# Kernel optimization log

Measured on AMD Instinct MI355X. Metric: run time of the kernel, lower is better.

## Reference

```python
import jax, jax.numpy as jnp
import numpy as np

N = 32768          # total proposals (batch of images concatenated)
C = 81             # num classes (class 0 = background)
K = 4096           # fixed candidate budget for masked NMS (jit-friendly)
SCORE_THRESH = 0.05
NMS_THRESH = 0.5
IMG_W, IMG_H = 1333.0, 800.0   # image size for clip_to_image
CLS_OFFSET = 4096.0            # > max coord: offsets boxes per label so NMS is per-class


def setup_inputs() -> dict:
    key = jax.random.key(0)
    k1, k2, k3 = jax.random.split(key, 3)
    x = jax.random.normal(k1, (N, C), dtype=jnp.float32)
    xy = jax.random.uniform(k2, (N, 2), dtype=jnp.float32) * jnp.array([IMG_W * 0.9, IMG_H * 0.9], jnp.float32)
    wh = 4.0 + jax.random.uniform(k3, (N, 2), dtype=jnp.float32) * 124.0
    boxes = jnp.concatenate([xy, xy + wh], axis=-1)  # [N,4] xyxy
    return {"x": x, "boxes": boxes}


def _pairwise_iou(b):
    # b: [K,4] xyxy -> [K,K] IoU
    x1, y1, x2, y2 = b[:, 0], b[:, 1], b[:, 2], b[:, 3]
    area = (x2 - x1) * (y2 - y1)
    iw = jnp.maximum(jnp.minimum(x2[:, None], x2[None, :]) - jnp.maximum(x1[:, None], x1[None, :]), 0.0)
    ih = jnp.maximum(jnp.minimum(y2[:, None], y2[None, :]) - jnp.maximum(y1[:, None], y1[None, :]), 0.0)
    inter = iw * ih
    return inter / (area[:, None] + area[None, :] - inter + 1e-9)


def reference(x, boxes):
    # softmax scores
    prob = jax.nn.softmax(x, axis=-1)                    # [N,C]
    # clip_to_image (remove_empty=False)
    bx = jnp.stack([
        jnp.clip(boxes[:, 0], 0.0, IMG_W - 1),
        jnp.clip(boxes[:, 1], 0.0, IMG_H - 1),
        jnp.clip(boxes[:, 2], 0.0, IMG_W - 1),
        jnp.clip(boxes[:, 3], 0.0, IMG_H - 1)], axis=-1)  # [N,4]
    # score threshold + drop background (label 0), as in filter_results
    valid = (prob > SCORE_THRESH) & (jnp.arange(C)[None, :] != 0)
    flat = jnp.where(valid, prob, -1.0).reshape(-1)       # [N*C]
    vals, idx = jax.lax.top_k(flat, K)                    # sorted desc
    box_idx = idx // C
    labels = idx % C                                      # [K] int
    bk = bx[box_idx]                                      # [K,4] (boxes repeated per class in torch code)
    keep0 = vals > 0.0                                    # invalid slots padded with -1
    # multi-label NMS: offset boxes by label so different classes never overlap
    boff = bk + (labels.astype(bk.dtype) * CLS_OFFSET)[:, None]
    iou_gt = _pairwise_iou(boff) > NMS_THRESH             # [K,K] bool
    order = jnp.arange(K)

    def step(keep, i):
        sup = keep[i] & (order > i) & iou_gt[i]
        return keep & ~sup, None

    keep, _ = jax.lax.scan(step, keep0, order)
    dets = jnp.where(keep[:, None],
                     jnp.concatenate([bk, vals[:, None]], axis=-1),
                     0.0)                                 # [K,5] = xyxy + score
    return dets, labels, keep
```

## Files before the change

kernel.cpp:

```cpp
#include <hip/hip_runtime.h>

#pragma clang fp contract(off)

typedef unsigned int u32;
typedef unsigned long long u64;
typedef long long i64;

#define N_ROWS 32768
#define NCLS 81
#define TOPK 4096
#define MAXCAND 327680
#define SELCAP 12288
#define IMGW_M1 1332.0f
#define IMGH_M1 799.0f

#define CAND_THREADS 256
#define RPB 32
#define CAND_GRID (N_ROWS / RPB)
#define CPT 11
#define BLK_CAND_CAP 640
#define ROW_F4 ((RPB * NCLS) / 4)

#define H1_BASE 0x3D4Cu
#define H1_BINS 576
#define H1_SLICES 64

#define COLL_GRID 512
#define SEG_LDS 4096

#define MCAP 1024
#define MMAX 512
#define NW32 16

__device__ inline double fast_exp_neg(double d) {
    if (d < -45.0) return 0.0;
    const double L2E    = 1.4426950408889634074;
    const double LN2_HI = 6.93147180369123816490e-01;
    const double LN2_LO = 1.90821492927058770002e-10;
    double n = __builtin_rint(d * L2E);
    double r = __builtin_fma(-n, LN2_HI, d);
    r = __builtin_fma(-n, LN2_LO, r);
    double p = 1.0 / 6227020800.0;
    p = __builtin_fma(p, r, 1.0 / 479001600.0);
    p = __builtin_fma(p, r, 1.0 / 39916800.0);
    p = __builtin_fma(p, r, 1.0 / 3628800.0);
    p = __builtin_fma(p, r, 1.0 / 362880.0);
    p = __builtin_fma(p, r, 1.0 / 40320.0);
    p = __builtin_fma(p, r, 1.0 / 5040.0);
    p = __builtin_fma(p, r, 1.0 / 720.0);
    p = __builtin_fma(p, r, 1.0 / 120.0);
    p = __builtin_fma(p, r, 1.0 / 24.0);
    p = __builtin_fma(p, r, 1.0 / 6.0);
    p = __builtin_fma(p, r, 0.5);
    p = __builtin_fma(p, r, 1.0);
    p = __builtin_fma(p, r, 1.0);
    i64 ni = (i64)n;
    double sc = __longlong_as_double((i64)(1023 + ni) << 52);
    return p * sc;
}

__global__ void __launch_bounds__(256) k_cand(const float* __restrict__ x,
                                              u32* __restrict__ candKey,
                                              u32* __restrict__ candIdx,
                                              u32* __restrict__ cnt,
                                              u32* __restrict__ hist1p) {
    __shared__ float4 lx4[ROW_F4];
    __shared__ u32 lK[BLK_CAND_CAP];
    __shared__ u32 lI[BLK_CAND_CAP];
    __shared__ u32 lh[H1_BINS];
    __shared__ u32 lcnt;
    __shared__ u32 gbaseSh;
    float* lx = (float*)lx4;
    const int t = threadIdx.x;
    if (t == 0) lcnt = 0;
    for (int i = t; i < H1_BINS; i += CAND_THREADS) lh[i] = 0;

    const float4* xv = (const float4*)x + (size_t)blockIdx.x * ROW_F4;
    for (int i = t; i < ROW_F4; i += CAND_THREADS) lx4[i] = xv[i];
    __syncthreads();

    const int rl = t >> 3;
    const int q = t & 7;
    const int c0 = q * 10;
    const int cEff = (q == 7) ? 11 : 10;
    const int row = blockIdx.x * RPB + rl;
    const float* xr = lx + rl * NCLS;

    float v[CPT];
    #pragma unroll
    for (int i = 0; i < CPT; i++) v[i] = (i < cEff) ? xr[c0 + i] : -1.0e30f;

    float m = v[0];
    #pragma unroll
    for (int i = 1; i < CPT; i++) m = fmaxf(m, v[i]);
    m = fmaxf(m, __shfl_xor(m, 1));
    m = fmaxf(m, __shfl_xor(m, 2));
    m = fmaxf(m, __shfl_xor(m, 4));

    double e[CPT];
    #pragma unroll
    for (int i = 0; i < CPT; i++) {
        if (i < cEff) {
            float d = v[i] - m;
            e[i] = fast_exp_neg((double)d);
        } else e[i] = 0.0;
    }
    double s = 0.0;
    #pragma unroll
    for (int i = 0; i < CPT; i++) if (i < cEff) s += e[i];
    s += __shfl_xor(s, 1);
    s += __shfl_xor(s, 2);
    s += __shfl_xor(s, 4);

    const double THRMID = (double)0.05f + 0x1.0p-29;
    double ethr = THRMID * s;
    #pragma unroll
    for (int i = 0; i < CPT; i++) {
        int c = c0 + i;
        if (i < cEff && c != 0 && e[i] > ethr) {
            float pf = (float)(e[i] / s);
            u32 slot = atomicAdd(&lcnt, 1u);
            lK[slot] = __float_as_uint(pf);
            lI[slot] = (u32)(row * NCLS + c);
        }
    }
    __syncthreads();
    u32 tot = lcnt;
    if (t == 0) gbaseSh = tot ? atomicAdd(&cnt[0], tot) : 0u;
    for (u32 i = t; i < tot; i += CAND_THREADS) {
        u32 b = (lK[i] >> 16) - H1_BASE;
        if (b < (u32)H1_BINS) atomicAdd(&lh[b], 1u);
    }
    __syncthreads();
    u32 gbase = gbaseSh;
    for (u32 i = t; i < tot; i += CAND_THREADS) {
        u32 g = gbase + i;
        if (g < MAXCAND) {
            candKey[g] = lK[i];
            candIdx[g] = lI[i];
        }
    }
    u32 ob = (blockIdx.x & (H1_SLICES - 1)) * H1_BINS;
    for (int i = t; i < H1_BINS; i += CAND_THREADS) {
        u32 h = lh[i];
        if (h) atomicAdd(&hist1p[ob + i], h);
    }
}

__global__ void __launch_bounds__(1024) k_midlite(const u32* __restrict__ hist1p,
                                                  u32* __restrict__ cnt,
                                                  u32* __restrict__ sufG) {
    __shared__ u32 cs[1024];
    int t = threadIdx.x;
    u32 s1 = 0;
    if (t < H1_BINS) {
        for (int j = 0; j < H1_SLICES; j++) s1 += hist1p[j * H1_BINS + t];
    }
    cs[t] = (t < H1_BINS) ? s1 : 0u;
    __syncthreads();
    for (int d = 1; d < 1024; d <<= 1) {
        u32 v = (t + d < 1024) ? cs[t + d] : 0u;
        __syncthreads();
        cs[t] += v;
        __syncthreads();
    }
    if (t < 577) sufG[t] = cs[t];
    u32 S_t = cs[t];
    u32 S_next = (t < 1023) ? cs[t + 1] : 0u;
    if (S_next < TOPK && S_t >= TOPK) cnt[3] = (u32)t;
}

__global__ void __launch_bounds__(256) k_collect(const u32* __restrict__ candKey,
                                                 const u32* __restrict__ candIdx,
                                                 u32* __restrict__ cnt,
                                                 const u32* __restrict__ sufG,
                                                 u32* __restrict__ binCur,
                                                 u64* __restrict__ sel) {
    u32 n = cnt[0] < (u32)MAXCAND ? cnt[0] : (u32)MAXCAND;
    u32 B = cnt[3];
    u32 stride = COLL_GRID * 256;
    for (u32 i = blockIdx.x * 256 + threadIdx.x; i < n; i += stride) {
        u32 k = candKey[i];
        u32 b = (k >> 16) - H1_BASE;
        if (b < (u32)H1_BINS && b >= B) {
            u32 pos = sufG[b + 1] + atomicAdd(&binCur[b], 1u);
            if (pos < (u32)SELCAP)
                sel[pos] = ((u64)k << 32) | (u64)(0xFFFFFFFFu - candIdx[i]);
        }
    }
}

__global__ void __launch_bounds__(256) k_binrank(const u64* __restrict__ sel,
                                                 const u32* __restrict__ cnt,
                                                 const u32* __restrict__ sufG,
                                                 const float* __restrict__ boxes,
                                                 float* __restrict__ rboxes,
                                                 float* __restrict__ rvals,
                                                 int* __restrict__ rlabel,
                                                 float* __restrict__ out) {
    const int t = threadIdx.x;
    const u32 B = cnt[3];

    if (blockIdx.x == H1_BINS) {
        u32 covered = sufG[B];
        if (covered > (u32)TOPK) covered = TOPK;
        for (u32 r = covered + t; r < TOPK; r += 256) {
            rboxes[r * 4 + 0] = 0; rboxes[r * 4 + 1] = 0;
            rboxes[r * 4 + 2] = 0; rboxes[r * 4 + 3] = 0;
            rvals[r] = 0.0f; rlabel[r] = 0;
            out[TOPK * 5 + r] = 0.0f;
            out[TOPK * 6 + r] = 0.0f;
            float* d = out + (size_t)r * 5;
            d[0] = 0; d[1] = 0; d[2] = 0; d[3] = 0; d[4] = 0;
        }
        return;
    }

    __shared__ u64 seg[SEG_LDS];
    const u32 b = blockIdx.x;
    if (b < B) return;
    u32 start = sufG[b + 1];
    u32 end = sufG[b];
    if (end > (u32)SELCAP) end = SELCAP;
    if (start >= end) return;
    u32 len = end - start;
    if (start >= (u32)TOPK) return;
    u32 ldsLen = len < (u32)SEG_LDS ? len : (u32)SEG_LDS;
    for (u32 i = t; i < ldsLen; i += 256) seg[i] = sel[start + i];
    __syncthreads();
    for (u32 i = t; i < len; i += 256) {
        u64 c = (i < ldsLen) ? seg[i] : sel[start + i];
        u32 r0 = 0;
        for (u32 j = 0; j < ldsLen; j++) r0 += (seg[j] > c) ? 1u : 0u;
        for (u32 j = ldsLen; j < len; j++) r0 += (sel[start + j] > c) ? 1u : 0u;
        u32 r = start + r0;
        if (r >= (u32)TOPK) continue;
        u32 idx = 0xFFFFFFFFu - (u32)(c & 0xFFFFFFFFull);
        float val = __uint_as_float((u32)(c >> 32));
        u32 bi = idx / NCLS;
        u32 lab = idx % NCLS;
        const float* bp = boxes + (size_t)bi * 4;
        float x1 = fminf(fmaxf(bp[0], 0.0f), IMGW_M1);
        float y1 = fminf(fmaxf(bp[1], 0.0f), IMGH_M1);
        float x2 = fminf(fmaxf(bp[2], 0.0f), IMGW_M1);
        float y2 = fminf(fmaxf(bp[3], 0.0f), IMGH_M1);
        rboxes[r * 4 + 0] = x1; rboxes[r * 4 + 1] = y1;
        rboxes[r * 4 + 2] = x2; rboxes[r * 4 + 3] = y2;
        rvals[r] = val;
        rlabel[r] = (int)lab;
        out[TOPK * 5 + r] = (float)lab;
    }
}

__device__ inline float4 nms_box(u32 g, const float4* __restrict__ boxL,
                                 const float* __restrict__ rboxes,
                                 const unsigned short* __restrict__ memRank, float off) {
    if (g < (u32)MCAP) return boxL[g];
    float4 b = ((const float4*)rboxes)[memRank[g]];
    return make_float4(b.x + off, b.y + off, b.z + off, b.w + off);
}
__device__ inline float nms_area(u32 g, const float* __restrict__ areaL, float4 b) {
    if (g < (u32)MCAP) return areaL[g];
    return (b.z - b.x) * (b.w - b.y);
}

__global__ void __launch_bounds__(256) k_nms(const float* __restrict__ rboxes,
                                             const float* __restrict__ rvals,
                                             const int* __restrict__ rlabel,
                                             float* __restrict__ out) {
    int c = blockIdx.x + 1;
    __shared__ int lLab[TOPK];
    __shared__ float4 boxL[MCAP];
    __shared__ float areaL[MCAP];
    __shared__ unsigned short memRank[TOPK];
    __shared__ u32 colW[MMAX * NW32];
    __shared__ u32 remOut[NW32];
    __shared__ unsigned char keepL[TOPK];
    __shared__ u32 cc[64];
    __shared__ u32 baseC[64];
    __shared__ u32 mTotSh;
    const int t = threadIdx.x;
    const int w = t >> 6, lane = t & 63;
    const u64 laneLT = ((u64)1 << lane) - 1;
    const float off = (float)c * 4096.0f;

    {
        const int4* g4 = (const int4*)rlabel;
        int4* l4 = (int4*)lLab;
        for (int i = t; i < TOPK / 4; i += 256) l4[i] = g4[i];
    }
    __syncthreads();

    for (int it = 0; it < 16; it++) {
        int chunk = it * 4 + w;
        int r = chunk * 64 + lane;
        u64 mask = __ballot(lLab[r] == c);
        if (lane == 0) cc[chunk] = (u32)__popcll(mask);
    }
    __syncthreads();
    if (t < 64) {
        u32 v = cc[t];
        u32 inc = v;
        #pragma unroll
        for (int d = 1; d < 64; d <<= 1) {
            u32 o = __shfl_up(inc, d);
            if (lane >= d) inc += o;
        }
        baseC[t] = inc - v;
        if (t == 63) mTotSh = inc;
    }
    __syncthreads();
    const u32 m = mTotSh;
    for (int it = 0; it < 16; it++) {
        int chunk = it * 4 + w;
        int r = chunk * 64 + lane;
        bool match = (lLab[r] == c);
        u64 mask = __ballot(match);
        if (match) {
            u32 g = baseC[chunk] + (u32)__popcll(mask & laneLT);
            memRank[g] = (unsigned short)r;
            if (g < (u32)MCAP) {
                float4 b = ((const float4*)rboxes)[r];
                float bx1 = b.x + off, by1 = b.y + off;
                float bx2 = b.z + off, by2 = b.w + off;
                boxL[g] = make_float4(bx1, by1, bx2, by2);
                areaL[g] = (bx2 - bx1) * (by2 - by1);
            }
        }
    }
    __syncthreads();

    const bool matrixPath = (m <= (u32)MMAX);
    if (matrixPath) {
        const u32 nW = (m + 31) >> 5;
        const u32 items = m * nW;
        for (u32 p = t; p < items; p += 256) {
            u32 s = p / nW;
            u32 wd = p - s * nW;
            float4 bs = nms_box(s, boxL, rboxes, memRank, off);
            float as = nms_area(s, areaL, bs);
            u32 word = 0;
            u32 j0 = wd << 5;
            u32 jend = j0 + 32; if (jend > m) jend = m;
            u32 js = (j0 > s + 1) ? j0 : (s + 1);
            for (u32 j = js; j < jend; j++) {
                float4 bj = nms_box(j, boxL, rboxes, memRank, off);
                float aj = nms_area(j, areaL, bj);
                float iw = fmaxf(fminf(bs.z, bj.z) - fmaxf(bs.x, bj.x), 0.0f);
                float ih = fmaxf(fminf(bs.w, bj.w) - fmaxf(bs.y, bj.y), 0.0f);
                float inter = iw * ih;
                float iou = inter / (as + aj - inter + 1e-9f);
                if (iou > 0.5f) word |= (1u << (j - j0));
            }
            colW[s * NW32 + wd] = word;
        }
        __syncthreads();
        if (t < 64) {
            u32 remW = 0;
            bool own = ((u32)lane < ((m + 31) >> 5));
            for (u32 s2 = 0; s2 < m; s2++) {
                u32 rw = __shfl(remW, (int)(s2 >> 5));
                bool removed = (rw >> (s2 & 31)) & 1u;
                u32 cw = own ? colW[s2 * NW32 + lane] : 0u;
                if (!removed) remW |= cw;
            }
            if (own) remOut[lane] = remW;
        }
        __syncthreads();
    } else {
        for (u32 q2 = t; q2 < m; q2 += 256) keepL[q2] = 1;
        __syncthreads();
        for (u32 i = 0; i < m; i++) {
            __syncthreads();
            if (!keepL[i]) continue;
            float4 bi = nms_box(i, boxL, rboxes, memRank, off);
            float ai = nms_area(i, areaL, bi);
            for (u32 jj = i + 1 + t; jj < m; jj += 256) {
                if (!keepL[jj]) continue;
                float4 bj = nms_box(jj, boxL, rboxes, memRank, off);
                float aj = nms_area(jj, areaL, bj);
                float iw = fmaxf(fminf(bi.z, bj.z) - fmaxf(bi.x, bj.x), 0.0f);
                float ih = fmaxf(fminf(bi.w, bj.w) - fmaxf(bi.y, bj.y), 0.0f);
                float inter = iw * ih;
                float iou = inter / (ai + aj - inter + 1e-9f);
                if (iou > 0.5f) keepL[jj] = 0;
            }
        }
        __syncthreads();
    }

    for (u32 q2 = t; q2 < m; q2 += 256) {
        bool keep = matrixPath ? !((remOut[q2 >> 5] >> (q2 & 31)) & 1u)
                               : (keepL[q2] != 0);
        int r = memRank[q2];
        out[TOPK * 6 + r] = keep ? 1.0f : 0.0f;
        float* d = out + (size_t)r * 5;
        if (keep) {
            float4 b = ((const float4*)rboxes)[r];
            d[0] = b.x; d[1] = b.y; d[2] = b.z; d[3] = b.w;
            d[4] = rvals[r];
        } else {
            d[0] = 0; d[1] = 0; d[2] = 0; d[3] = 0; d[4] = 0;
        }
    }
}

extern "C" void kernel_launch(void* const* d_in, const int* in_sizes, int n_in,
                              void* d_out, int out_size, void* d_ws, size_t ws_size,
                              hipStream_t stream) {
    const float* x = (const float*)d_in[0];
    const float* boxes = (const float*)d_in[1];
    float* out = (float*)d_out;

    u32* W = (u32*)d_ws;
    u32* cnt = W;
    u32* hist1p = W + 16;
    u32* binCur = W + 16 + 36864;
    u32* sufG = binCur + 576;
    u32* candKey = sufG + 584;
    u32* candIdx = candKey + MAXCAND;
    u64* sel = (u64*)(candIdx + MAXCAND);
    float* rboxes = (float*)(sel + SELCAP);
    float* rvals = rboxes + 4 * TOPK;
    int* rlabel = (int*)(rvals + TOPK);

    hipMemsetAsync(W, 0, (16 + 36864 + 576) * sizeof(u32), stream);
    k_cand<<<CAND_GRID, CAND_THREADS, 0, stream>>>(x, candKey, candIdx, cnt, hist1p);
    k_midlite<<<1, 1024, 0, stream>>>(hist1p, cnt, sufG);
    k_collect<<<COLL_GRID, 256, 0, stream>>>(candKey, candIdx, cnt, sufG, binCur, sel);
    k_binrank<<<H1_BINS + 1, 256, 0, stream>>>(sel, cnt, sufG, boxes,
                                               rboxes, rvals, rlabel, out);
    k_nms<<<80, 256, 0, stream>>>(rboxes, rvals, rlabel, out);
}
```

Measured before the change: 115.0 us.

## Fuse histogram scan and candidate collection into per-bin rank kernel

After: 158.3 us. 1.38x slower.

```diff
diff --git a/kernel.cpp b/kernel.cpp
--- a/kernel.cpp
+++ b/kernel.cpp
@@ -10,7 +10,6 @@
 #define NCLS 81
 #define TOPK 4096
 #define MAXCAND 327680
-#define SELCAP 12288
 #define IMGW_M1 1332.0f
 #define IMGH_M1 799.0f
 
@@ -25,7 +24,6 @@
 #define H1_BINS 576
 #define H1_SLICES 64
 
-#define COLL_GRID 512
 #define SEG_LDS 4096
 
 #define MCAP 1024
@@ -147,62 +145,62 @@
     }
 }
 
-__global__ void __launch_bounds__(1024) k_midlite(const u32* __restrict__ hist1p,
-                                                  u32* __restrict__ cnt,
-                                                  u32* __restrict__ sufG) {
-    __shared__ u32 cs[1024];
-    int t = threadIdx.x;
-    u32 s1 = 0;
-    if (t < H1_BINS) {
-        for (int j = 0; j < H1_SLICES; j++) s1 += hist1p[j * H1_BINS + t];
-    }
-    cs[t] = (t < H1_BINS) ? s1 : 0u;
-    __syncthreads();
-    for (int d = 1; d < 1024; d <<= 1) {
-        u32 v = (t + d < 1024) ? cs[t + d] : 0u;
-        __syncthreads();
-        cs[t] += v;
-        __syncthreads();
-    }
-    if (t < 577) sufG[t] = cs[t];
-    u32 S_t = cs[t];
-    u32 S_next = (t < 1023) ? cs[t + 1] : 0u;
-    if (S_next < TOPK && S_t >= TOPK) cnt[3] = (u32)t;
-}
-
-__global__ void __launch_bounds__(256) k_collect(const u32* __restrict__ candKey,
+__global__ void __launch_bounds__(256) k_binrank(const u32* __restrict__ candKey,
                                                  const u32* __restrict__ candIdx,
-                                                 u32* __restrict__ cnt,
-                                                 const u32* __restrict__ sufG,
-                                                 u32* __restrict__ binCur,
-                                                 u64* __restrict__ sel) {
-    u32 n = cnt[0] < (u32)MAXCAND ? cnt[0] : (u32)MAXCAND;
-    u32 B = cnt[3];
-    u32 stride = COLL_GRID * 256;
-    for (u32 i = blockIdx.x * 256 + threadIdx.x; i < n; i += stride) {
-        u32 k = candKey[i];
-        u32 b = (k >> 16) - H1_BASE;
-        if (b < (u32)H1_BINS && b >= B) {
-            u32 pos = sufG[b + 1] + atomicAdd(&binCur[b], 1u);
-            if (pos < (u32)SELCAP)
-                sel[pos] = ((u64)k << 32) | (u64)(0xFFFFFFFFu - candIdx[i]);
-        }
-    }
-}
-
-__global__ void __launch_bounds__(256) k_binrank(const u64* __restrict__ sel,
                                                  const u32* __restrict__ cnt,
-                                                 const u32* __restrict__ sufG,
+                                                 const u32* __restrict__ hist1p,
                                                  const float* __restrict__ boxes,
                                                  float* __restrict__ rboxes,
                                                  float* __restrict__ rvals,
                                                  int* __restrict__ rlabel,
                                                  float* __restrict__ out) {
+    __shared__ u32 cs[1024];
+    __shared__ u64 seg[SEG_LDS];
+    __shared__ u32 scnt;
+    __shared__ u32 Bsh;
     const int t = threadIdx.x;
-    const u32 B = cnt[3];
+
+    if (t == 0) { scnt = 0; Bsh = 0; }
+
+    {
+        u32 s0 = 0, s1 = 0, s2 = 0;
+        const bool g1 = (t + 256) < H1_BINS;
+        const bool g2 = (t + 512) < H1_BINS;
+        for (int j = 0; j < H1_SLICES; j++) {
+            const u32* hp = hist1p + j * H1_BINS;
+            s0 += hp[t];
+            if (g1) s1 += hp[t + 256];
+            if (g2) s2 += hp[t + 512];
+        }
+        cs[t] = s0;
+        cs[t + 256] = g1 ? s1 : 0u;
+        cs[t + 512] = g2 ? s2 : 0u;
+        cs[t + 768] = 0u;
+    }
+    __syncthreads();
+    for (int d = 1; d < 1024; d <<= 1) {
+        u32 a0 = (t + d < 1024) ? cs[t + d] : 0u;
+        u32 a1 = (t + 256 + d < 1024) ? cs[t + 256 + d] : 0u;
+        u32 a2 = (t + 512 + d < 1024) ? cs[t + 512 + d] : 0u;
+        u32 a3 = (t + 768 + d < 1024) ? cs[t + 768 + d] : 0u;
+        __syncthreads();
+        cs[t] += a0; cs[t + 256] += a1; cs[t + 512] += a2; cs[t + 768] += a3;
+        __syncthreads();
+    }
+    #pragma unroll
+    for (int qq = 0; qq < 3; qq++) {
+        int i = t + qq * 256;
+        if (i < H1_BINS) {
+            u32 S_t = cs[i];
+            u32 S_n = cs[i + 1];
+            if (S_t >= (u32)TOPK && S_n < (u32)TOPK) Bsh = (u32)i;
+        }
+    }
+    __syncthreads();
+    const u32 B = Bsh;
 
     if (blockIdx.x == H1_BINS) {
-        u32 covered = sufG[B];
+        u32 covered = cs[B];
         if (covered > (u32)TOPK) covered = TOPK;
         for (u32 r = covered + t; r < TOPK; r += 256) {
             rboxes[r * 4 + 0] = 0; rboxes[r * 4 + 1] = 0;
@@ -216,39 +214,92 @@
         return;
     }
 
-    __shared__ u64 seg[SEG_LDS];
     const u32 b = blockIdx.x;
     if (b < B) return;
-    u32 start = sufG[b + 1];
-    u32 end = sufG[b];
-    if (end > (u32)SELCAP) end = SELCAP;
+    u32 start = cs[b + 1];
+    u32 end = cs[b];
     if (start >= end) return;
-    u32 len = end - start;
     if (start >= (u32)TOPK) return;
-    u32 ldsLen = len < (u32)SEG_LDS ? len : (u32)SEG_LDS;
-    for (u32 i = t; i < ldsLen; i += 256) seg[i] = sel[start + i];
-    __syncthreads();
-    for (u32 i = t; i < len; i += 256) {
-        u64 c = (i < ldsLen) ? seg[i] : sel[start + i];
-        u32 r0 = 0;
-        for (u32 j = 0; j < ldsLen; j++) r0 += (seg[j] > c) ? 1u : 0u;
-        for (u32 j = ldsLen; j < len; j++) r0 += (sel[start + j] > c) ? 1u : 0u;
-        u32 r = start + r0;
-        if (r >= (u32)TOPK) continue;
-        u32 idx = 0xFFFFFFFFu - (u32)(c & 0xFFFFFFFFull);
-        float val = __uint_as_float((u32)(c >> 32));
-        u32 bi = idx / NCLS;
-        u32 lab = idx % NCLS;
-        const float* bp = boxes + (size_t)bi * 4;
-        float x1 = fminf(fmaxf(bp[0], 0.0f), IMGW_M1);
-        float y1 = fminf(fmaxf(bp[1], 0.0f), IMGH_M1);
-        float x2 = fminf(fmaxf(bp[2], 0.0f), IMGW_M1);
-        float y2 = fminf(fmaxf(bp[3], 0.0f), IMGH_M1);
-        rboxes[r * 4 + 0] = x1; rboxes[r * 4 + 1] = y1;
-        rboxes[r * 4 + 2] = x2; rboxes[r * 4 + 3] = y2;
-        rvals[r] = val;
-        rlabel[r] = (int)lab;
-        out[TOPK * 5 + r] = (float)lab;
+
+    u32 n = cnt[0];
+    if (n > (u32)MAXCAND) n = MAXCAND;
+    u32 n4 = n & ~3u;
+    for (u32 i0 = (u32)t * 4u; i0 < n4; i0 += 1024u) {
+        const uint4 k4 = *reinterpret_cast<const uint4*>(candKey + i0);
+        u32 ks[4] = { k4.x, k4.y, k4.z, k4.w };
+        #pragma unroll
+        for (int e2 = 0; e2 < 4; e2++) {
+            u32 k = ks[e2];
+            if (((k >> 16) - H1_BASE) == b) {
+                u32 slot = atomicAdd(&scnt, 1u);
+                if (slot < (u32)SEG_LDS)
+                    seg[slot] = ((u64)k << 32) | (u64)(0xFFFFFFFFu - candIdx[i0 + (u32)e2]);
+            }
+        }
+    }
+    for (u32 i = n4 + (u32)t; i < n; i += 256u) {
+        u32 k = candKey[i];
+        if (((k >> 16) - H1_BASE) == b) {
+            u32 slot = atomicAdd(&scnt, 1u);
+            if (slot < (u32)SEG_LDS)
+                seg[slot] = ((u64)k << 32) | (u64)(0xFFFFFFFFu - candIdx[i]);
+        }
+    }
+    __syncthreads();
+    const u32 len = scnt;
+
+    if (len <= (u32)SEG_LDS) {
+        for (u32 i = t; i < len; i += 256) {
+            u64 c = seg[i];
+            u32 r0 = 0;
+            for (u32 j = 0; j < len; j++) r0 += (seg[j] > c) ? 1u : 0u;
+            u32 r = start + r0;
+            if (r >= (u32)TOPK) continue;
+            u32 idx = 0xFFFFFFFFu - (u32)(c & 0xFFFFFFFFull);
+            float val = __uint_as_float((u32)(c >> 32));
+            u32 bi = idx / NCLS;
+            u32 lab = idx % NCLS;
+            const float* bp = boxes + (size_t)bi * 4;
+            float x1 = fminf(fmaxf(bp[0], 0.0f), IMGW_M1);
+            float y1 = fminf(fmaxf(bp[1], 0.0f), IMGH_M1);
+            float x2 = fminf(fmaxf(bp[2], 0.0f), IMGW_M1);
+            float y2 = fminf(fmaxf(bp[3], 0.0f), IMGH_M1);
+            rboxes[r * 4 + 0] = x1; rboxes[r * 4 + 1] = y1;
+            rboxes[r * 4 + 2] = x2; rboxes[r * 4 + 3] = y2;
+            rvals[r] = val;
+            rlabel[r] = (int)lab;
+            out[TOPK * 5 + r] = (float)lab;
+        }
+    } else {
+        for (u32 i = t; i < n; i += 256) {
+            u32 k = candKey[i];
+            if (((k >> 16) - H1_BASE) != b) continue;
+            u64 c = ((u64)k << 32) | (u64)(0xFFFFFFFFu - candIdx[i]);
+            u32 r0 = 0;
+            for (u32 j = 0; j < n; j++) {
+                u32 k2 = candKey[j];
+                if (((k2 >> 16) - H1_BASE) == b) {
+                    u64 c2 = ((u64)k2 << 32) | (u64)(0xFFFFFFFFu - candIdx[j]);
+                    r0 += (c2 > c) ? 1u : 0u;
+                }
+            }
+            u32 r = start + r0;
+            if (r >= (u32)TOPK) continue;
+            u32 idx = 0xFFFFFFFFu - (u32)(c & 0xFFFFFFFFull);
+            float val = __uint_as_float((u32)(c >> 32));
+            u32 bi = idx / NCLS;
+            u32 lab = idx % NCLS;
+            const float* bp = boxes + (size_t)bi * 4;
+            float x1 = fminf(fmaxf(bp[0], 0.0f), IMGW_M1);
+            float y1 = fminf(fmaxf(bp[1], 0.0f), IMGH_M1);
+            float x2 = fminf(fmaxf(bp[2], 0.0f), IMGW_M1);
+            float y2 = fminf(fmaxf(bp[3], 0.0f), IMGH_M1);
+            rboxes[r * 4 + 0] = x1; rboxes[r * 4 + 1] = y1;
+            rboxes[r * 4 + 2] = x2; rboxes[r * 4 + 3] = y2;
+            rvals[r] = val;
+            rlabel[r] = (int)lab;
+            out[TOPK * 5 + r] = (float)lab;
+        }
     }
 }
 
@@ -415,20 +466,15 @@
     u32* W = (u32*)d_ws;
     u32* cnt = W;
     u32* hist1p = W + 16;
-    u32* binCur = W + 16 + 36864;
-    u32* sufG = binCur + 576;
-    u32* candKey = sufG + 584;
+    u32* candKey = W + 16 + 36864;
     u32* candIdx = candKey + MAXCAND;
-    u64* sel = (u64*)(candIdx + MAXCAND);
-    float* rboxes = (float*)(sel + SELCAP);
+    float* rboxes = (float*)(candIdx + MAXCAND);
     float* rvals = rboxes + 4 * TOPK;
     int* rlabel = (int*)(rvals + TOPK);
 
-    hipMemsetAsync(W, 0, (16 + 36864 + 576) * sizeof(u32), stream);
+    hipMemsetAsync(W, 0, (16 + 36864) * sizeof(u32), stream);
     k_cand<<<CAND_GRID, CAND_THREADS, 0, stream>>>(x, candKey, candIdx, cnt, hist1p);
-    k_midlite<<<1, 1024, 0, stream>>>(hist1p, cnt, sufG);
-    k_collect<<<COLL_GRID, 256, 0, stream>>>(candKey, candIdx, cnt, sufG, binCur, sel);
-    k_binrank<<<H1_BINS + 1, 256, 0, stream>>>(sel, cnt, sufG, boxes,
+    k_binrank<<<H1_BINS + 1, 256, 0, stream>>>(candKey, candIdx, cnt, hist1p, boxes,
                                                rboxes, rvals, rlabel, out);
     k_nms<<<80, 256, 0, stream>>>(rboxes, rvals, rlabel, out);
 }
```

## Scatter candidates directly into per-bin buckets, drop histogram and collect passes

Applied to the files above, without the earlier changes.

Result: slower. 257.7 us (+124.2%).

```diff
diff --git a/kernel.cpp b/kernel.cpp
--- a/kernel.cpp
+++ b/kernel.cpp
@@ -9,8 +9,6 @@
 #define N_ROWS 32768
 #define NCLS 81
 #define TOPK 4096
-#define MAXCAND 327680
-#define SELCAP 12288
 #define IMGW_M1 1332.0f
 #define IMGH_M1 799.0f
 
@@ -18,14 +16,12 @@
 #define RPB 32
 #define CAND_GRID (N_ROWS / RPB)
 #define CPT 11
-#define BLK_CAND_CAP 640
 #define ROW_F4 ((RPB * NCLS) / 4)
 
 #define H1_BASE 0x3D4Cu
 #define H1_BINS 576
-#define H1_SLICES 64
-
-#define COLL_GRID 512
+
+#define BCAP 6144
 #define SEG_LDS 4096
 
 #define MCAP 1024
@@ -60,20 +56,11 @@
 }
 
 __global__ void __launch_bounds__(256) k_cand(const float* __restrict__ x,
-                                              u32* __restrict__ candKey,
-                                              u32* __restrict__ candIdx,
-                                              u32* __restrict__ cnt,
-                                              u32* __restrict__ hist1p) {
+                                              u32* __restrict__ binCur,
+                                              u64* __restrict__ selBins) {
     __shared__ float4 lx4[ROW_F4];
-    __shared__ u32 lK[BLK_CAND_CAP];
-    __shared__ u32 lI[BLK_CAND_CAP];
-    __shared__ u32 lh[H1_BINS];
-    __shared__ u32 lcnt;
-    __shared__ u32 gbaseSh;
     float* lx = (float*)lx4;
     const int t = threadIdx.x;
-    if (t == 0) lcnt = 0;
-    for (int i = t; i < H1_BINS; i += CAND_THREADS) lh[i] = 0;
 
     const float4* xv = (const float4*)x + (size_t)blockIdx.x * ROW_F4;
     for (int i = t; i < ROW_F4; i += CAND_THREADS) lx4[i] = xv[i];
@@ -119,90 +106,61 @@
         int c = c0 + i;
         if (i < cEff && c != 0 && e[i] > ethr) {
             float pf = (float)(e[i] / s);
-            u32 slot = atomicAdd(&lcnt, 1u);
-            lK[slot] = __float_as_uint(pf);
-            lI[slot] = (u32)(row * NCLS + c);
-        }
-    }
-    __syncthreads();
-    u32 tot = lcnt;
-    if (t == 0) gbaseSh = tot ? atomicAdd(&cnt[0], tot) : 0u;
-    for (u32 i = t; i < tot; i += CAND_THREADS) {
-        u32 b = (lK[i] >> 16) - H1_BASE;
-        if (b < (u32)H1_BINS) atomicAdd(&lh[b], 1u);
-    }
-    __syncthreads();
-    u32 gbase = gbaseSh;
-    for (u32 i = t; i < tot; i += CAND_THREADS) {
-        u32 g = gbase + i;
-        if (g < MAXCAND) {
-            candKey[g] = lK[i];
-            candIdx[g] = lI[i];
-        }
-    }
-    u32 ob = (blockIdx.x & (H1_SLICES - 1)) * H1_BINS;
-    for (int i = t; i < H1_BINS; i += CAND_THREADS) {
-        u32 h = lh[i];
-        if (h) atomicAdd(&hist1p[ob + i], h);
-    }
-}
-
-__global__ void __launch_bounds__(1024) k_midlite(const u32* __restrict__ hist1p,
-                                                  u32* __restrict__ cnt,
-                                                  u32* __restrict__ sufG) {
-    __shared__ u32 cs[1024];
-    int t = threadIdx.x;
-    u32 s1 = 0;
-    if (t < H1_BINS) {
-        for (int j = 0; j < H1_SLICES; j++) s1 += hist1p[j * H1_BINS + t];
-    }
-    cs[t] = (t < H1_BINS) ? s1 : 0u;
-    __syncthreads();
-    for (int d = 1; d < 1024; d <<= 1) {
-        u32 v = (t + d < 1024) ? cs[t + d] : 0u;
-        __syncthreads();
-        cs[t] += v;
-        __syncthreads();
-    }
-    if (t < 577) sufG[t] = cs[t];
-    u32 S_t = cs[t];
-    u32 S_next = (t < 1023) ? cs[t + 1] : 0u;
-    if (S_next < TOPK && S_t >= TOPK) cnt[3] = (u32)t;
-}
-
-__global__ void __launch_bounds__(256) k_collect(const u32* __restrict__ candKey,
-                                                 const u32* __restrict__ candIdx,
-                                                 u32* __restrict__ cnt,
-                                                 const u32* __restrict__ sufG,
-                                                 u32* __restrict__ binCur,
-                                                 u64* __restrict__ sel) {
-    u32 n = cnt[0] < (u32)MAXCAND ? cnt[0] : (u32)MAXCAND;
-    u32 B = cnt[3];
-    u32 stride = COLL_GRID * 256;
-    for (u32 i = blockIdx.x * 256 + threadIdx.x; i < n; i += stride) {
-        u32 k = candKey[i];
-        u32 b = (k >> 16) - H1_BASE;
-        if (b < (u32)H1_BINS && b >= B) {
-            u32 pos = sufG[b + 1] + atomicAdd(&binCur[b], 1u);
-            if (pos < (u32)SELCAP)
-                sel[pos] = ((u64)k << 32) | (u64)(0xFFFFFFFFu - candIdx[i]);
-        }
-    }
-}
-
-__global__ void __launch_bounds__(256) k_binrank(const u64* __restrict__ sel,
-                                                 const u32* __restrict__ cnt,
-                                                 const u32* __restrict__ sufG,
+            u32 key = __float_as_uint(pf);
+            u32 b = (key >> 16) - H1_BASE;
+            u32 pos = atomicAdd(&binCur[b], 1u);
+            if (pos < (u32)BCAP)
+                selBins[(size_t)b * BCAP + pos] =
+                    ((u64)key << 32) | (u64)(0xFFFFFFFFu - (u32)(row * NCLS + c));
+        }
+    }
+}
+
+__global__ void __launch_bounds__(256) k_binrank(const u64* __restrict__ selBins,
+                                                 const u32* __restrict__ binCur,
                                                  const float* __restrict__ boxes,
                                                  float* __restrict__ rboxes,
                                                  float* __restrict__ rvals,
                                                  int* __restrict__ rlabel,
                                                  float* __restrict__ out) {
+    __shared__ u32 cs[1040];
+    __shared__ u64 seg[SEG_LDS];
+    __shared__ u32 Bsh;
     const int t = threadIdx.x;
-    const u32 B = cnt[3];
+
+    if (t == 0) Bsh = 0;
+
+    {
+        u32 s0 = binCur[t];
+        u32 s1 = ((t + 256) < H1_BINS) ? binCur[t + 256] : 0u;
+        u32 s2 = ((t + 512) < H1_BINS) ? binCur[t + 512] : 0u;
+        cs[t] = s0;
+        cs[t + 256] = s1;
+        cs[t + 512] = s2;
+        cs[t + 768] = 0u;
+    }
+    __syncthreads();
+    for (int d = 1; d < 1024; d <<= 1) {
+        u32 a0 = (t + d < 1024) ? cs[t + d] : 0u;
+        u32 a1 = (t + 256 + d < 1024) ? cs[t + 256 + d] : 0u;
+        u32 a2 = (t + 512 + d < 1024) ? cs[t + 512 + d] : 0u;
+        u32 a3 = (t + 768 + d < 1024) ? cs[t + 768 + d] : 0u;
+        __syncthreads();
+        cs[t] += a0; cs[t + 256] += a1; cs[t + 512] += a2; cs[t + 768] += a3;
+        __syncthreads();
+    }
+    #pragma unroll
+    for (int qq = 0; qq < 3; qq++) {
+        int i = t + qq * 256;
+        if (i < H1_BINS) {
+            if (cs[i] >= (u32)TOPK && cs[i + 1] < (u32)TOPK) Bsh = (u32)i;
+        }
+    }
+    __syncthreads();
+    const u32 B = Bsh;
 
     if (blockIdx.x == H1_BINS) {
-        u32 covered = sufG[B];
+        u32 covered = cs[B];
         if (covered > (u32)TOPK) covered = TOPK;
         for (u32 r = covered + t; r < TOPK; r += 256) {
             rboxes[r * 4 + 0] = 0; rboxes[r * 4 + 1] = 0;
@@ -216,23 +174,24 @@
         return;
     }
 
-    __shared__ u64 seg[SEG_LDS];
     const u32 b = blockIdx.x;
     if (b < B) return;
-    u32 start = sufG[b + 1];
-    u32 end = sufG[b];
-    if (end > (u32)SELCAP) end = SELCAP;
+    u32 start = cs[b + 1];
+    u32 end = cs[b];
     if (start >= end) return;
-    u32 len = end - start;
     if (start >= (u32)TOPK) return;
-    u32 ldsLen = len < (u32)SEG_LDS ? len : (u32)SEG_LDS;
-    for (u32 i = t; i < ldsLen; i += 256) seg[i] = sel[start + i];
-    __syncthreads();
-    for (u32 i = t; i < len; i += 256) {
-        u64 c = (i < ldsLen) ? seg[i] : sel[start + i];
+
+    u32 lenTrue = end - start;
+    u32 lenSt = lenTrue < (u32)BCAP ? lenTrue : (u32)BCAP;
+    u32 ldsLen = lenSt < (u32)SEG_LDS ? lenSt : (u32)SEG_LDS;
+    const u64* gseg = selBins + (size_t)b * BCAP;
+    for (u32 i = t; i < ldsLen; i += 256) seg[i] = gseg[i];
+    __syncthreads();
+    for (u32 i = t; i < lenSt; i += 256) {
+        u64 c = (i < ldsLen) ? seg[i] : gseg[i];
         u32 r0 = 0;
         for (u32 j = 0; j < ldsLen; j++) r0 += (seg[j] > c) ? 1u : 0u;
-        for (u32 j = ldsLen; j < len; j++) r0 += (sel[start + j] > c) ? 1u : 0u;
+        for (u32 j = ldsLen; j < lenSt; j++) r0 += (gseg[j] > c) ? 1u : 0u;
         u32 r = start + r0;
         if (r >= (u32)TOPK) continue;
         u32 idx = 0xFFFFFFFFu - (u32)(c & 0xFFFFFFFFull);
@@ -413,22 +372,15 @@
     float* out = (float*)d_out;
 
     u32* W = (u32*)d_ws;
-    u32* cnt = W;
-    u32* hist1p = W + 16;
-    u32* binCur = W + 16 + 36864;
-    u32* sufG = binCur + 576;
-    u32* candKey = sufG + 584;
-    u32* candIdx = candKey + MAXCAND;
-    u64* sel = (u64*)(candIdx + MAXCAND);
-    float* rboxes = (float*)(sel + SELCAP);
+    u32* binCur = W;
+    u64* selBins = (u64*)((char*)d_ws + 4096);
+    float* rboxes = (float*)(selBins + (size_t)H1_BINS * BCAP);
     float* rvals = rboxes + 4 * TOPK;
     int* rlabel = (int*)(rvals + TOPK);
 
-    hipMemsetAsync(W, 0, (16 + 36864 + 576) * sizeof(u32), stream);
-    k_cand<<<CAND_GRID, CAND_THREADS, 0, stream>>>(x, candKey, candIdx, cnt, hist1p);
-    k_midlite<<<1, 1024, 0, stream>>>(hist1p, cnt, sufG);
-    k_collect<<<COLL_GRID, 256, 0, stream>>>(candKey, candIdx, cnt, sufG, binCur, sel);
-    k_binrank<<<H1_BINS + 1, 256, 0, stream>>>(sel, cnt, sufG, boxes,
+    hipMemsetAsync(binCur, 0, H1_BINS * sizeof(u32), stream);
+    k_cand<<<CAND_GRID, CAND_THREADS, 0, stream>>>(x, binCur, selBins);
+    k_binrank<<<H1_BINS + 1, 256, 0, stream>>>(selBins, binCur, boxes,
                                                rboxes, rvals, rlabel, out);
     k_nms<<<80, 256, 0, stream>>>(rboxes, rvals, rlabel, out);
 }
```
